# Kernel tuning notes

Hardware: AMD Instinct MI355X
Metric: run time of the kernel (lower is better)

The kernel has to match this reference:

```python
import jax, jax.numpy as jnp
import numpy as np

N = 100000   # nodes
E = 300000   # edges
D = 256      # emb_dim
L = 5        # num_layers
SELF_LOOP_BOND_TYPE = 4
BN_EPS = 1e-5


def setup_inputs() -> dict:
    key = jax.random.key(0)
    ks = jax.random.split(key, 12)
    s = 0.05
    x = jax.random.randint(ks[0], (N, 2), 0, 3)
    edge_index = jax.random.randint(ks[1], (2, E), 0, N)
    edge_attr = jax.random.randint(ks[2], (E, 2), 0, 3)
    x_emb1 = jax.random.normal(ks[3], (120, D), dtype=jnp.float32) * s
    x_emb2 = jax.random.normal(ks[4], (3, D), dtype=jnp.float32) * s
    edge_emb1 = jax.random.normal(ks[5], (L, 6, D), dtype=jnp.float32) * s
    edge_emb2 = jax.random.normal(ks[6], (L, 3, D), dtype=jnp.float32) * s
    W1 = jax.random.normal(ks[7], (L, D, 2 * D), dtype=jnp.float32) * (1.0 / np.sqrt(D))
    b1 = jnp.zeros((L, 2 * D), dtype=jnp.float32)
    W2 = jax.random.normal(ks[8], (L, 2 * D, D), dtype=jnp.float32) * (1.0 / np.sqrt(2 * D))
    b2 = jnp.zeros((L, D), dtype=jnp.float32)
    bn_gamma = jnp.ones((L - 1, D), dtype=jnp.float32)
    bn_beta = jnp.zeros((L - 1, D), dtype=jnp.float32)
    return dict(x=x, edge_index=edge_index, edge_attr=edge_attr,
                x_emb1=x_emb1, x_emb2=x_emb2,
                edge_emb1=edge_emb1, edge_emb2=edge_emb2,
                W1=W1, b1=b1, W2=W2, b2=b2,
                bn_gamma=bn_gamma, bn_beta=bn_beta)


def reference(x, edge_index, edge_attr, x_emb1, x_emb2, edge_emb1, edge_emb2,
              W1, b1, W2, b2, bn_gamma, bn_beta):
    n = x.shape[0]
    loop = jnp.arange(n)
    # add_self_loops: append (i, i) for every node
    src = jnp.concatenate([edge_index[0], loop])  # [E+N]
    dst = jnp.concatenate([edge_index[1], loop])  # [E+N]
    # self-loop edge_attr = (bond_type=4, direction=0)
    self_attr = jnp.concatenate([
        jnp.full((n, 1), SELF_LOOP_BOND_TYPE, dtype=edge_attr.dtype),
        jnp.zeros((n, 1), dtype=edge_attr.dtype)], axis=1)
    ea = jnp.concatenate([edge_attr, self_attr], axis=0)  # [E+N, 2]

    out = x_emb1[x[:, 0]] + x_emb2[x[:, 1]]  # [N, D]
    for l in range(L):
        e_emb = edge_emb1[l][ea[:, 0]] + edge_emb2[l][ea[:, 1]]  # [E+N, D]
        msg = out[src] + e_emb                                   # gather + message
        agg = jax.ops.segment_sum(msg, dst, num_segments=n)      # scatter-add
        h = jax.nn.relu(agg @ W1[l] + b1[l]) @ W2[l] + b2[l]     # GIN MLP
        if l < L - 1:
            mean = h.mean(axis=0)
            var = h.var(axis=0)  # biased var, matches torch BN training
            h = (h - mean) * jax.lax.rsqrt(var + BN_EPS) * bn_gamma[l] + bn_beta[l]
            h = jax.nn.relu(h)
        out = h
    return out
```

## Files before the change

kernel.cpp:

```cpp
#include <hip/hip_runtime.h>

typedef unsigned short u16;
typedef unsigned int u32;

#define DD 256

typedef short  s16x8 __attribute__((ext_vector_type(8)));
typedef short  s16x4 __attribute__((ext_vector_type(4)));
typedef float  f32x4 __attribute__((ext_vector_type(4)));
typedef float  f32x16 __attribute__((ext_vector_type(16)));

__device__ __forceinline__ float b2f(u16 u){
  union { u32 i; float f; } c; c.i = ((u32)u) << 16; return c.f;
}
__device__ __forceinline__ u16 f2b(float f){
  union { float f; u32 i; } c; c.f = f;
  u32 b = c.i + 0x7FFFu + ((c.i >> 16) & 1u);
  return (u16)(b >> 16);
}

__global__ void NodeEncoder_72971494359603_kernel(){}

__global__ void probe_dtype(const u32* w, u32* flag){
  if (threadIdx.x == 0 && blockIdx.x == 0){
    int cnt = 0;
    for (int i = 0; i < 256; i++){
      u32 low = w[i] & 0xFFFFu;
      u32 e = (low >> 7) & 0xFFu;
      if (e >= 0x60u && e <= 0x7Eu) cnt++;
    }
    *flag = (cnt >= 192) ? 1u : 0u;
  }
}

__global__ void cvt_in(const void* src, u16* dst, int n, const u32* flag){
  int i = blockIdx.x * 256 + threadIdx.x;
  if (i < n){
    if (*flag){
      dst[i] = ((const u16*)src)[i];
    } else {
      dst[i] = f2b(((const float*)src)[i]);
    }
  }
}

__global__ void store_out(const u16* h, void* dout, int n, const u32* flag){
  int i = blockIdx.x * 256 + threadIdx.x;
  if (i < n){
    if (*flag){
      ((u16*)dout)[i] = h[i];
    } else {
      ((float*)dout)[i] = b2f(h[i]);
    }
  }
}

__global__ void zero_int(int* p, int n){
  int i = blockIdx.x * 256 + threadIdx.x;
  if (i < n) p[i] = 0;
}

__global__ void build_table(const u16* ee1, const u16* ee2, u16* TBL){
  int b = blockIdx.x;
  int l = b / 18, c = b % 18, a = c / 3, bb = c % 3;
  int j = threadIdx.x;
  TBL[b * DD + j] = f2b(b2f(ee1[(l * 6 + a) * DD + j]) + b2f(ee2[(l * 3 + bb) * DD + j]));
}

__global__ void hist_kernel(const int* dst, int* counts, int E){
  int e = blockIdx.x * 256 + threadIdx.x;
  if (e < E) atomicAdd(&counts[dst[e]], 1);
}

__global__ void scan_sums(const int* counts, int* bsum, int N){
  __shared__ int red[256];
  int tid = threadIdx.x;
  int base = blockIdx.x * 1024;
  int s = 0;
  for (int i = tid; i < 1024; i += 256){
    int g = base + i;
    if (g < N) s += counts[g];
  }
  red[tid] = s;
  __syncthreads();
  for (int off = 128; off > 0; off >>= 1){
    if (tid < off) red[tid] += red[tid + off];
    __syncthreads();
  }
  if (tid == 0) bsum[blockIdx.x] = red[0];
}

__global__ void scan_top(int* bsum, int nb){
  if (threadIdx.x == 0 && blockIdx.x == 0){
    int acc = 0;
    for (int i = 0; i < nb; i++){ int t = bsum[i]; bsum[i] = acc; acc += t; }
  }
}

__global__ void scan_block(const int* counts, const int* bsum,
                           int* offsets, int* cursor, int N){
  __shared__ int tsum[256];
  int b = blockIdx.x;
  int tid = threadIdx.x;
  int base = b * 1024;
  int v0, v1, v2, v3;
  int g = base + tid * 4;
  v0 = (g + 0 < N) ? counts[g + 0] : 0;
  v1 = (g + 1 < N) ? counts[g + 1] : 0;
  v2 = (g + 2 < N) ? counts[g + 2] : 0;
  v3 = (g + 3 < N) ? counts[g + 3] : 0;
  tsum[tid] = v0 + v1 + v2 + v3;
  __syncthreads();
  for (int off = 1; off < 256; off <<= 1){
    int t = (tid >= off) ? tsum[tid - off] : 0;
    __syncthreads();
    tsum[tid] += t;
    __syncthreads();
  }
  int excl = (tid == 0 ? 0 : tsum[tid - 1]) + bsum[b];
  if (g + 0 < N){ offsets[g + 0] = excl; cursor[g + 0] = excl; } excl += v0;
  if (g + 1 < N){ offsets[g + 1] = excl; cursor[g + 1] = excl; } excl += v1;
  if (g + 2 < N){ offsets[g + 2] = excl; cursor[g + 2] = excl; } excl += v2;
  if (g + 3 < N){ offsets[g + 3] = excl; cursor[g + 3] = excl; }
}

__global__ void fill_csr(const int* ei, const int* ea, int* cursor,
                         int* payload, int E){
  int e = blockIdx.x * 256 + threadIdx.x;
  if (e < E){
    int d = ei[E + e];
    int pos = atomicAdd(&cursor[d], 1);
    int a = ea[2 * e], bb = ea[2 * e + 1];
    payload[pos] = ei[e] | ((a * 3 + bb) << 17);
  }
}

__global__ void node_embed(const int* x, const u16* xe1, const u16* xe2,
                           u16* out, int N){
  int idx = blockIdx.x * 256 + threadIdx.x;
  if (idx < N * DD){
    int n = idx >> 8, j = idx & 255;
    int x0 = x[2 * n], x1 = x[2 * n + 1];
    out[idx] = f2b(b2f(xe1[x0 * DD + j]) + b2f(xe2[x1 * DD + j]));
  }
}

__global__ void pack_B(const u16* __restrict__ W0, u16* __restrict__ Wp0, int K, int Nc){
  const u16* W = W0 + (size_t)blockIdx.y * K * Nc;
  u16* Wp = Wp0 + (size_t)blockIdx.y * K * Nc;
  int idx = blockIdx.x * 256 + threadIdx.x;
  int lane = idx & 63;
  int t = idx >> 6;
  int nk = K >> 4;
  int kstep = t % nk, cblk = t / nk;
  if (cblk >= (Nc >> 5)) return;
  int col = cblk * 32 + (lane & 31);
  int krow = kstep * 16 + (lane >> 5) * 8;
  u16* dst = Wp + (size_t)idx * 8;
#pragma unroll
  for (int e = 0; e < 8; e++)
    dst[e] = W[(size_t)(krow + e) * Nc + col];
}

__global__ __launch_bounds__(512, 4)
void layer_fused(const u16* __restrict__ feat, const u16* __restrict__ TBL,
                 const int* __restrict__ offsets, const int* __restrict__ counts,
                 const int* __restrict__ payload,
                 const u16* __restrict__ Wp1, const u16* __restrict__ bias1,
                 const u16* __restrict__ Wp2, const u16* __restrict__ bias2,
                 u16* __restrict__ H, float* __restrict__ partial, int npart, int M,
                 const float* __restrict__ sums, const u16* __restrict__ gamma,
                 const u16* __restrict__ beta, float invN, int apply_bn){
  __shared__ __align__(16) u16 As[64 * 256];
  __shared__ __align__(16) u16 Ms[2][64 * 128];
  u16* T = (u16*)Ms;
  int tid = threadIdx.x, lane = tid & 63, wave = tid >> 6;
  int wr = wave >> 2, wc = wave & 3;
  int row0 = blockIdx.x * 64;
  int l31 = lane & 31, lhi = lane >> 5;

  {
    u32* Tw = (u32*)T;
    const u32* Gw = (const u32*)TBL;
    for (int i = tid; i < 18 * DD / 2; i += 512) Tw[i] = Gw[i];
  }
  __syncthreads();

  {
    int c4 = lane * 4;
    float sc[4], sh[4];
    if (apply_bn){
#pragma unroll
      for (int e = 0; e < 4; e++){
        int j = c4 + e;
        float mean = sums[j] * invN;
        float var = sums[DD + j] * invN - mean * mean;
        if (var < 0.f) var = 0.f;
        float scl = rsqrtf(var + 1e-5f) * b2f(gamma[j]);
        sc[e] = scl; sh[e] = b2f(beta[j]) - mean * scl;
      }
    } else {
#pragma unroll
      for (int e = 0; e < 4; e++){ sc[e] = 1.f; sh[e] = 0.f; }
    }
    for (int u = 0; u < 8; u++){
      int r = wave * 8 + u;
      int n = row0 + r; if (n > M - 1) n = M - 1;
      s16x4 sv = *(const s16x4*)(feat + (size_t)n * DD + c4);
      s16x4 tb = *(const s16x4*)(T + 12 * DD + c4);
      float v0 = b2f((u16)sv[0]) * sc[0] + sh[0];
      float v1 = b2f((u16)sv[1]) * sc[1] + sh[1];
      float v2 = b2f((u16)sv[2]) * sc[2] + sh[2];
      float v3 = b2f((u16)sv[3]) * sc[3] + sh[3];
      if (apply_bn){
        v0 = fmaxf(v0, 0.f); v1 = fmaxf(v1, 0.f);
        v2 = fmaxf(v2, 0.f); v3 = fmaxf(v3, 0.f);
      }
      float a0 = v0 + b2f((u16)tb[0]);
      float a1 = v1 + b2f((u16)tb[1]);
      float a2 = v2 + b2f((u16)tb[2]);
      float a3 = v3 + b2f((u16)tb[3]);
      int e0 = offsets[n], eend = e0 + counts[n];
      for (int e = e0; e < eend; e += 4){
        int nb = eend - e; if (nb > 4) nb = 4;
        int pls[4]; s16x4 rvs[4]; s16x4 tvs[4];
#pragma unroll
        for (int i = 0; i < 4; i++)
          if (i < nb) pls[i] = payload[e + i];
#pragma unroll
        for (int i = 0; i < 4; i++)
          if (i < nb){
            rvs[i] = *(const s16x4*)(feat + (size_t)(pls[i] & 0x1FFFF) * DD + c4);
            tvs[i] = *(const s16x4*)(T + (pls[i] >> 17) * DD + c4);
          }
#pragma unroll
        for (int i = 0; i < 4; i++)
          if (i < nb){
            float w0 = b2f((u16)rvs[i][0]) * sc[0] + sh[0];
            float w1 = b2f((u16)rvs[i][1]) * sc[1] + sh[1];
            float w2 = b2f((u16)rvs[i][2]) * sc[2] + sh[2];
            float w3 = b2f((u16)rvs[i][3]) * sc[3] + sh[3];
            if (apply_bn){
              w0 = fmaxf(w0, 0.f); w1 = fmaxf(w1, 0.f);
              w2 = fmaxf(w2, 0.f); w3 = fmaxf(w3, 0.f);
            }
            a0 += w0 + b2f((u16)tvs[i][0]);
            a1 += w1 + b2f((u16)tvs[i][1]);
            a2 += w2 + b2f((u16)tvs[i][2]);
            a3 += w3 + b2f((u16)tvs[i][3]);
          }
      }
      s16x4 o;
      o[0] = (short)f2b(a0); o[1] = (short)f2b(a1);
      o[2] = (short)f2b(a2); o[3] = (short)f2b(a3);
      int byteo = r * 512 + (((lane >> 1) ^ (r & 31)) << 4) + ((lane & 1) << 3);
      *(s16x4*)((char*)As + byteo) = o;
    }
  }
  __syncthreads();

  f32x16 acc2[2];
#pragma unroll
  for (int n = 0; n < 2; n++)
#pragma unroll
    for (int i = 0; i < 16; i++) acc2[n][i] = 0.f;
  f32x16 acc1;

  auto G1 = [&](int cc){
    f32x16 a1;
#pragma unroll
    for (int i = 0; i < 16; i++) a1[i] = 0.f;
    int arow = wr * 32 + l31;
    int cb = cc * 4 + wc;
#pragma unroll
    for (int ks = 0; ks < 16; ks++){
      int slot = (ks * 2 + lhi) ^ (arow & 31);
      s16x8 af = *(const s16x8*)((const char*)As + arow * 512 + (slot << 4));
      s16x8 bf = *(const s16x8*)(Wp1 + (((size_t)cb * 16 + ks) * 64 + lane) * 8);
      a1 = __builtin_amdgcn_mfma_f32_32x32x16_bf16(af, bf, a1, 0, 0, 0);
    }
    acc1 = a1;
  };
  auto WMS = [&](int cc, int buf){
    char* ms = (char*)Ms[buf];
    int col = wc * 32 + l31;
    float bv = b2f(bias1[cc * 128 + col]);
#pragma unroll
    for (int reg = 0; reg < 16; reg++){
      int mrow = wr * 32 + (reg & 3) + 8 * (reg >> 2) + 4 * lhi;
      float v = fmaxf(acc1[reg] + bv, 0.f);
      int slot = (col >> 3) ^ (mrow & 15);
      *(u16*)(ms + mrow * 256 + (slot << 4) + (col & 7) * 2) = f2b(v);
    }
  };

  G1(0);
  WMS(0, 0);
  __syncthreads();

#pragma unroll
  for (int c = 0; c < 4; c++){
    const char* ms = (const char*)Ms[c & 1];
    int mrow = wr * 32 + l31;
#pragma unroll
    for (int ks = 0; ks < 8; ks++){
      int slot = (ks * 2 + lhi) ^ (mrow & 15);
      s16x8 mf = *(const s16x8*)(ms + mrow * 256 + (slot << 4));
#pragma unroll
      for (int n = 0; n < 2; n++){
        int cb2 = wc * 2 + n;
        s16x8 wf = *(const s16x8*)(Wp2 + (((size_t)cb2 * 32 + c * 8 + ks) * 64 + lane) * 8);
        acc2[n] = __builtin_amdgcn_mfma_f32_32x32x16_bf16(mf, wf, acc2[n], 0, 0, 0);
      }
    }
    if (c < 3){
      G1(c + 1);
      WMS(c + 1, (c + 1) & 1);
      __syncthreads();
    }
  }

#pragma unroll
  for (int n = 0; n < 2; n++){
    int col = wc * 64 + n * 32 + l31;
    float bv = b2f(bias2[col]);
#pragma unroll
    for (int reg = 0; reg < 16; reg++){
      int row = wr * 32 + (reg & 3) + 8 * (reg >> 2) + 4 * lhi;
      int slot = (col >> 3) ^ (row & 31);
      *(u16*)((char*)As + row * 512 + (slot << 4) + (col & 7) * 2) = f2b(acc2[n][reg] + bv);
    }
  }
  __syncthreads();

  float s[8], q[8];
#pragma unroll
  for (int e = 0; e < 8; e++){ s[e] = 0.f; q[e] = 0.f; }
  int sl = tid & 31;
#pragma unroll
  for (int p = 0; p < 4; p++){
    int r = p * 16 + (tid >> 5);
    s16x8 v = *(const s16x8*)((const char*)As + r * 512 + ((sl ^ (r & 31)) << 4));
    int gr = row0 + r;
    if (gr < M){
      *(s16x8*)(H + (size_t)gr * DD + sl * 8) = v;
      if (partial){
#pragma unroll
        for (int e = 0; e < 8; e++){
          float f = b2f((u16)v[e]);
          s[e] += f; q[e] += f * f;
        }
      }
    }
  }
  if (partial){
#pragma unroll
    for (int e = 0; e < 8; e++){
      s[e] += __shfl_xor(s[e], 32);
      q[e] += __shfl_xor(q[e], 32);
    }
    __syncthreads();
    float* redS = (float*)Ms;
    float* redQ = redS + 8 * 256;
    if (lane < 32){
#pragma unroll
      for (int e = 0; e < 8; e++){
        redS[wave * 256 + sl * 8 + e] = s[e];
        redQ[wave * 256 + sl * 8 + e] = q[e];
      }
    }
    __syncthreads();
    if (tid < 256){
      float a = 0.f, b = 0.f;
#pragma unroll
      for (int w = 0; w < 8; w++){ a += redS[w * 256 + tid]; b += redQ[w * 256 + tid]; }
      partial[(size_t)blockIdx.x * DD + tid] = a;
      partial[(size_t)(npart + blockIdx.x) * DD + tid] = b;
    }
  }
}

__global__ void bn_reduce(const float* __restrict__ partial, float* __restrict__ sums,
                          int npart){
  int b = blockIdx.x, which = b >> 3, jg = b & 7;
  int t = threadIdx.x;
  int j = jg * 32 + (t >> 3);
  int li = t & 7;
  float s = 0.f;
  for (int i = li; i < npart; i += 8)
    s += partial[(size_t)(which * npart + i) * DD + j];
  s += __shfl_xor(s, 1); s += __shfl_xor(s, 2); s += __shfl_xor(s, 4);
  if (li == 0) sums[which * DD + j] = s;
}

extern "C" void kernel_launch(void* const* d_in, const int* in_sizes, int n_in,
                              void* d_out, int out_size, void* d_ws, size_t ws_size,
                              hipStream_t stream){
  (void)n_in; (void)out_size; (void)ws_size;
  const int* x    = (const int*)d_in[0];
  const int* ei   = (const int*)d_in[1];
  const int* ea   = (const int*)d_in[2];
  const void* xe1 = d_in[3];
  const void* xe2 = d_in[4];
  const void* ee1 = d_in[5];
  const void* ee2 = d_in[6];
  const void* W1  = d_in[7];
  const void* b1  = d_in[8];
  const void* W2  = d_in[9];
  const void* b2  = d_in[10];
  const void* gam = d_in[11];
  const void* bet = d_in[12];

  int N = in_sizes[0] / 2;
  int E = in_sizes[1] / 2;
  int NB = (N + 1023) / 1024;
  const int L = 5;
  int nblk = (N + 63) / 64;
  int npart = nblk;

  char* base = (char*)d_ws;
  size_t off = 0;
  u32* flag    = (u32*)(base + off);   off += 256;
  u16* TBL     = (u16*)(base + off);   off += ((size_t)L * 18 * DD * 2 + 255) & ~(size_t)255;
  int* counts  = (int*)(base + off);   off += ((size_t)N * 4 + 255) & ~(size_t)255;
  int* offsets = (int*)(base + off);   off += ((size_t)N * 4 + 255) & ~(size_t)255;
  int* cursor  = (int*)(base + off);   off += ((size_t)N * 4 + 255) & ~(size_t)255;
  int* bsum    = (int*)(base + off);   off += ((size_t)NB * 4 + 255) & ~(size_t)255;
  int* payload = (int*)(base + off);   off += ((size_t)E * 4 + 255) & ~(size_t)255;
  float* part  = (float*)(base + off); off += ((size_t)2 * npart * DD * 4 + 255) & ~(size_t)255;
  float* sums  = (float*)(base + off); off += ((size_t)2 * DD * 4 + 255) & ~(size_t)255;
  u16* wx1  = (u16*)(base + off); off += ((size_t)120 * DD * 2 + 255) & ~(size_t)255;
  u16* wx2  = (u16*)(base + off); off += ((size_t)3 * DD * 2 + 255) & ~(size_t)255;
  u16* wee1 = (u16*)(base + off); off += ((size_t)L * 6 * DD * 2 + 255) & ~(size_t)255;
  u16* wee2 = (u16*)(base + off); off += ((size_t)L * 3 * DD * 2 + 255) & ~(size_t)255;
  u16* wW1  = (u16*)(base + off); off += ((size_t)L * DD * 2 * DD * 2 + 255) & ~(size_t)255;
  u16* wb1  = (u16*)(base + off); off += ((size_t)L * 2 * DD * 2 + 255) & ~(size_t)255;
  u16* wW2  = (u16*)(base + off); off += ((size_t)L * 2 * DD * DD * 2 + 255) & ~(size_t)255;
  u16* wb2  = (u16*)(base + off); off += ((size_t)L * DD * 2 + 255) & ~(size_t)255;
  u16* wgam = (u16*)(base + off); off += ((size_t)(L - 1) * DD * 2 + 255) & ~(size_t)255;
  u16* wbet = (u16*)(base + off); off += ((size_t)(L - 1) * DD * 2 + 255) & ~(size_t)255;
  u16* Wp1  = (u16*)(base + off); off += ((size_t)L * DD * 2 * DD * 2 + 255) & ~(size_t)255;
  u16* Wp2  = (u16*)(base + off); off += ((size_t)L * 2 * DD * DD * 2 + 255) & ~(size_t)255;
  u16* featA = (u16*)(base + off); off += ((size_t)N * DD * 2 + 255) & ~(size_t)255;
  u16* featB = (u16*)(base + off); off += ((size_t)N * DD * 2 + 255) & ~(size_t)255;

  probe_dtype<<<1, 64, 0, stream>>>((const u32*)xe1, flag);
  cvt_in<<<(120 * DD + 255) / 256, 256, 0, stream>>>(xe1, wx1, 120 * DD, flag);
  cvt_in<<<(3 * DD + 255) / 256, 256, 0, stream>>>(xe2, wx2, 3 * DD, flag);
  cvt_in<<<(L * 6 * DD + 255) / 256, 256, 0, stream>>>(ee1, wee1, L * 6 * DD, flag);
  cvt_in<<<(L * 3 * DD + 255) / 256, 256, 0, stream>>>(ee2, wee2, L * 3 * DD, flag);
  cvt_in<<<(L * DD * 2 * DD + 255) / 256, 256, 0, stream>>>(W1, wW1, L * DD * 2 * DD, flag);
  cvt_in<<<(L * 2 * DD + 255) / 256, 256, 0, stream>>>(b1, wb1, L * 2 * DD, flag);
  cvt_in<<<(L * 2 * DD * DD + 255) / 256, 256, 0, stream>>>(W2, wW2, L * 2 * DD * DD, flag);
  cvt_in<<<(L * DD + 255) / 256, 256, 0, stream>>>(b2, wb2, L * DD, flag);
  cvt_in<<<((L - 1) * DD + 255) / 256, 256, 0, stream>>>(gam, wgam, (L - 1) * DD, flag);
  cvt_in<<<((L - 1) * DD + 255) / 256, 256, 0, stream>>>(bet, wbet, (L - 1) * DD, flag);

  build_table<<<90, 256, 0, stream>>>(wee1, wee2, TBL);
  pack_B<<<dim3(64, L), 256, 0, stream>>>(wW1, Wp1, DD, 2 * DD);
  pack_B<<<dim3(64, L), 256, 0, stream>>>(wW2, Wp2, 2 * DD, DD);
  zero_int<<<(N + 255) / 256, 256, 0, stream>>>(counts, N);
  hist_kernel<<<(E + 255) / 256, 256, 0, stream>>>(ei + E, counts, E);
  scan_sums<<<NB, 256, 0, stream>>>(counts, bsum, N);
  scan_top<<<1, 64, 0, stream>>>(bsum, NB);
  scan_block<<<NB, 256, 0, stream>>>(counts, bsum, offsets, cursor, N);
  fill_csr<<<(E + 255) / 256, 256, 0, stream>>>(ei, ea, cursor, payload, E);

  node_embed<<<(N * DD + 255) / 256, 256, 0, stream>>>(x, wx1, wx2, featA, N);

  float invN = 1.0f / (float)N;
  u16* fin = featA;
  u16* fout = featB;

  for (int l = 0; l < L; l++){
    layer_fused<<<nblk, 512, 0, stream>>>(
        fin, TBL + (size_t)l * 18 * DD, offsets, counts, payload,
        Wp1 + (size_t)l * DD * 2 * DD, wb1 + (size_t)l * 2 * DD,
        Wp2 + (size_t)l * 2 * DD * DD, wb2 + (size_t)l * DD,
        fout, (l < L - 1) ? part : (float*)nullptr, npart, N,
        sums, wgam + (size_t)(l > 0 ? l - 1 : 0) * DD,
        wbet + (size_t)(l > 0 ? l - 1 : 0) * DD, invN, l > 0 ? 1 : 0);

    if (l < L - 1){
      bn_reduce<<<16, 256, 0, stream>>>(part, sums, npart);
    }
    u16* t = fin; fin = fout; fout = t;
  }

  store_out<<<(N * DD + 255) / 256, 256, 0, stream>>>(fin, d_out, N * DD, flag);
}
```

Measured before the change: 1.604 ms.

## Stage edge payload in LDS and interleave two rows in gather loop

The block's CSR payload slice is prefetched cooperatively into shared memory, with a fallback to global memory past a cap. Offsets, counts and self features for all 8 rows of a wave are loaded up front. Two destination rows are then processed together so twice as many independent neighbor gathers are in flight. This targets gather latency and the dependent payload→feature load chain, at the cost of more registers and extra LDS traffic that could reduce occupancy.

```diff
diff --git a/kernel.cpp b/kernel.cpp
--- a/kernel.cpp
+++ b/kernel.cpp
@@ -4,6 +4,7 @@
 typedef unsigned int u32;
 
 #define DD 256
+#define PLCAP 1536
 
 typedef short  s16x8 __attribute__((ext_vector_type(8)));
 typedef short  s16x4 __attribute__((ext_vector_type(4)));
@@ -174,6 +175,7 @@
   __shared__ __align__(16) u16 As[64 * 256];
   __shared__ __align__(16) u16 Ms[2][64 * 128];
   u16* T = (u16*)Ms;
+  int* PL = (int*)((char*)Ms + 10240);
   int tid = threadIdx.x, lane = tid & 63, wave = tid >> 6;
   int wr = wave >> 2, wc = wave & 3;
   int row0 = blockIdx.x * 64;
@@ -184,6 +186,10 @@
     const u32* Gw = (const u32*)TBL;
     for (int i = tid; i < 18 * DD / 2; i += 512) Tw[i] = Gw[i];
   }
+  int nlast = row0 + 63; if (nlast > M - 1) nlast = M - 1;
+  int e_start = offsets[row0];
+  int e_total = offsets[nlast] + counts[nlast] - e_start;
+  for (int i = tid; i < e_total && i < PLCAP; i += 512) PL[i] = payload[e_start + i];
   __syncthreads();
 
   {
@@ -203,58 +209,85 @@
 #pragma unroll
       for (int e = 0; e < 4; e++){ sc[e] = 1.f; sh[e] = 0.f; }
     }
+    int rbase = wave * 8;
+    int offs[8], cnts[8]; s16x4 sv[8];
+#pragma unroll
     for (int u = 0; u < 8; u++){
-      int r = wave * 8 + u;
-      int n = row0 + r; if (n > M - 1) n = M - 1;
-      s16x4 sv = *(const s16x4*)(feat + (size_t)n * DD + c4);
-      s16x4 tb = *(const s16x4*)(T + 12 * DD + c4);
-      float v0 = b2f((u16)sv[0]) * sc[0] + sh[0];
-      float v1 = b2f((u16)sv[1]) * sc[1] + sh[1];
-      float v2 = b2f((u16)sv[2]) * sc[2] + sh[2];
-      float v3 = b2f((u16)sv[3]) * sc[3] + sh[3];
-      if (apply_bn){
-        v0 = fmaxf(v0, 0.f); v1 = fmaxf(v1, 0.f);
-        v2 = fmaxf(v2, 0.f); v3 = fmaxf(v3, 0.f);
-      }
-      float a0 = v0 + b2f((u16)tb[0]);
-      float a1 = v1 + b2f((u16)tb[1]);
-      float a2 = v2 + b2f((u16)tb[2]);
-      float a3 = v3 + b2f((u16)tb[3]);
-      int e0 = offsets[n], eend = e0 + counts[n];
-      for (int e = e0; e < eend; e += 4){
-        int nb = eend - e; if (nb > 4) nb = 4;
-        int pls[4]; s16x4 rvs[4]; s16x4 tvs[4];
+      int n = row0 + rbase + u; if (n > M - 1) n = M - 1;
+      offs[u] = offsets[n]; cnts[u] = counts[n];
+      sv[u] = *(const s16x4*)(feat + (size_t)n * DD + c4);
+    }
+    s16x4 tb = *(const s16x4*)(T + 12 * DD + c4);
+#pragma unroll
+    for (int up = 0; up < 4; up++){
+      float a0[4], a1[4];
+#pragma unroll
+      for (int h = 0; h < 2; h++){
+        float* a = h ? a1 : a0;
+        s16x4 svv = sv[up * 2 + h];
+#pragma unroll
+        for (int j = 0; j < 4; j++){
+          float v = b2f((u16)svv[j]) * sc[j] + sh[j];
+          if (apply_bn) v = fmaxf(v, 0.f);
+          a[j] = v + b2f((u16)tb[j]);
+        }
+      }
+      int e0 = offs[up * 2],     c0 = cnts[up * 2],     i0 = 0;
+      int e1 = offs[up * 2 + 1], c1 = cnts[up * 2 + 1], i1 = 0;
+      while (i0 < c0 || i1 < c1){
+        int b0 = c0 - i0; if (b0 > 4) b0 = 4; if (b0 < 0) b0 = 0;
+        int b1 = c1 - i1; if (b1 > 4) b1 = 4; if (b1 < 0) b1 = 0;
+        int pls0[4], pls1[4]; s16x4 rv0[4], rv1[4];
+#pragma unroll
+        for (int i = 0; i < 4; i++){
+          if (i < b0){
+            int idx = e0 + i0 + i - e_start;
+            pls0[i] = (idx < PLCAP) ? PL[idx] : payload[e0 + i0 + i];
+          }
+          if (i < b1){
+            int idx = e1 + i1 + i - e_start;
+            pls1[i] = (idx < PLCAP) ? PL[idx] : payload[e1 + i1 + i];
+          }
+        }
 #pragma unroll
         for (int i = 0; i < 4; i++)
-          if (i < nb) pls[i] = payload[e + i];
+          if (i < b0) rv0[i] = *(const s16x4*)(feat + (size_t)(pls0[i] & 0x1FFFF) * DD + c4);
 #pragma unroll
         for (int i = 0; i < 4; i++)
-          if (i < nb){
-            rvs[i] = *(const s16x4*)(feat + (size_t)(pls[i] & 0x1FFFF) * DD + c4);
-            tvs[i] = *(const s16x4*)(T + (pls[i] >> 17) * DD + c4);
+          if (i < b1) rv1[i] = *(const s16x4*)(feat + (size_t)(pls1[i] & 0x1FFFF) * DD + c4);
+#pragma unroll
+        for (int i = 0; i < 4; i++){
+          if (i < b0){
+            s16x4 tv = *(const s16x4*)(T + (pls0[i] >> 17) * DD + c4);
+#pragma unroll
+            for (int j = 0; j < 4; j++){
+              float w = b2f((u16)rv0[i][j]) * sc[j] + sh[j];
+              if (apply_bn) w = fmaxf(w, 0.f);
+              a0[j] += w + b2f((u16)tv[j]);
+            }
           }
-#pragma unroll
-        for (int i = 0; i < 4; i++)
-          if (i < nb){
-            float w0 = b2f((u16)rvs[i][0]) * sc[0] + sh[0];
-            float w1 = b2f((u16)rvs[i][1]) * sc[1] + sh[1];
-            float w2 = b2f((u16)rvs[i][2]) * sc[2] + sh[2];
-            float w3 = b2f((u16)rvs[i][3]) * sc[3] + sh[3];
-            if (apply_bn){
-              w0 = fmaxf(w0, 0.f); w1 = fmaxf(w1, 0.f);
-              w2 = fmaxf(w2, 0.f); w3 = fmaxf(w3, 0.f);
+          if (i < b1){
+            s16x4 tv = *(const s16x4*)(T + (pls1[i] >> 17) * DD + c4);
+#pragma unroll
+            for (int j = 0; j < 4; j++){
+              float w = b2f((u16)rv1[i][j]) * sc[j] + sh[j];
+              if (apply_bn) w = fmaxf(w, 0.f);
+              a1[j] += w + b2f((u16)tv[j]);
             }
-            a0 += w0 + b2f((u16)tvs[i][0]);
-            a1 += w1 + b2f((u16)tvs[i][1]);
-            a2 += w2 + b2f((u16)tvs[i][2]);
-            a3 += w3 + b2f((u16)tvs[i][3]);
           }
-      }
-      s16x4 o;
-      o[0] = (short)f2b(a0); o[1] = (short)f2b(a1);
-      o[2] = (short)f2b(a2); o[3] = (short)f2b(a3);
-      int byteo = r * 512 + (((lane >> 1) ^ (r & 31)) << 4) + ((lane & 1) << 3);
-      *(s16x4*)((char*)As + byteo) = o;
+        }
+        i0 += b0; i1 += b1;
+      }
+#pragma unroll
+      for (int h = 0; h < 2; h++){
+        float* a = h ? a1 : a0;
+        int r = rbase + up * 2 + h;
+        s16x4 o;
+        o[0] = (short)f2b(a[0]); o[1] = (short)f2b(a[1]);
+        o[2] = (short)f2b(a[2]); o[3] = (short)f2b(a[3]);
+        int byteo = r * 512 + (((lane >> 1) ^ (r & 31)) << 4) + ((lane & 1) << 3);
+        *(s16x4*)((char*)As + byteo) = o;
+      }
     }
   }
   __syncthreads();
```

Result: faster. 1.504 ms (-6.2%).
